# Performance work log

Hardware: AMD Instinct MI355X
Metric: run time of the kernel (lower is better)

## Reference

```python
import jax, jax.numpy as jnp
import numpy as np

B, N, D, E = 256, 192, 512, 1024
H = E // 2          # MLP hidden = 512
K = 58              # round(0.3 * 192), hardcoded in the torch forward
EPS_L2 = 1e-8
EPS_BN = 1e-5


def setup_inputs() -> dict:
    key = jax.random.key(0)
    ks = jax.random.split(key, 8)
    s = 0.02
    return {
        "all_patch_embeddings": jax.random.normal(ks[0], (B, N, D), dtype=jnp.float32),
        "attention_map": jax.random.uniform(ks[1], (B, N + 1, N + 1), dtype=jnp.float32),
        # fc: Linear(D, E)
        "W_fc": jax.random.normal(ks[2], (E, D), dtype=jnp.float32) * s,
        "b_fc": jnp.zeros((E,), dtype=jnp.float32),
        # mlp layer 0: Linear(D, H) + BatchNorm1d(H) + ReLU
        "W1": jax.random.normal(ks[3], (H, D), dtype=jnp.float32) * s,
        "b1": jnp.zeros((H,), dtype=jnp.float32),
        "gamma1": jnp.ones((H,), dtype=jnp.float32),
        "beta1": jnp.zeros((H,), dtype=jnp.float32),
        # mlp layer 1: Linear(H, E) (no BN/ReLU applied on last layer)
        "W2": jax.random.normal(ks[4], (E, H), dtype=jnp.float32) * s,
        "b2": jnp.zeros((E,), dtype=jnp.float32),
    }


def reference(all_patch_embeddings, attention_map, W_fc, b_fc, W1, b1, gamma1, beta1, W2, b2):
    # CLS-row attention over the 192 patch tokens: [B, N]
    cls_attn = attention_map[:, 0, 1:]
    # torch.sort(descending)[...,:K] == top-k indices (batched, replaces python loop)
    _, idx = jax.lax.top_k(cls_attn, K)                      # [B, K] int32
    # batched gather replacing the per-sample index_select loop
    sel = jnp.take_along_axis(all_patch_embeddings, idx[:, :, None], axis=1)  # [B, K, D]
    # l2norm over last dim
    norm = jnp.sqrt(jnp.sum(sel * sel, axis=-1, keepdims=True)) + EPS_L2
    base = sel / norm
    # .half() cast in the original (round-trip to fp16 precision)
    base = base.astype(jnp.float16).astype(jnp.float32)
    # fc branch
    feat_fc = jnp.einsum('bkd,ed->bke', base, W_fc) + b_fc    # [B, K, E]
    # mlp branch (num_layers=2): Linear -> BN(train-mode batch stats) -> ReLU -> Linear
    h = jnp.einsum('bkd,hd->bkh', base, W1) + b1              # [B, K, H]
    hf = h.reshape(B * K, H)
    mu = jnp.mean(hf, axis=0)
    var = jnp.var(hf, axis=0)
    hf = (hf - mu) * jax.lax.rsqrt(var + EPS_BN) * gamma1 + beta1
    h = jax.nn.relu(hf).reshape(B, K, H)
    feat_mlp = jnp.einsum('bkh,eh->bke', h, W2) + b2          # [B, K, E]
    feats = feat_mlp + feat_fc
    # maxk_pool1d_var with k=1 and lengths == K reduces to max over token dim
    return jnp.max(feats, axis=1).astype(jnp.float32)         # [B, E]
```

## Files before the change

kernel.cpp:

```cpp
#include <hip/hip_runtime.h>
#include <hip/hip_fp16.h>

#define B_ 256
#define N_ 192
#define D_ 512
#define E_ 1024
#define H_ 512
#define K_ 58
#define M_ (B_*K_)
#define M2_ (B_*64)

typedef _Float16 f16;
typedef unsigned int u32;
typedef _Float16 half8 __attribute__((ext_vector_type(8)));
typedef float floatx16 __attribute__((ext_vector_type(16)));

__device__ inline half8 cvt8(float4 f0, float4 f1) {
  half8 r;
  r[0]=(f16)f0.x; r[1]=(f16)f0.y; r[2]=(f16)f0.z; r[3]=(f16)f0.w;
  r[4]=(f16)f1.x; r[5]=(f16)f1.y; r[6]=(f16)f1.z; r[7]=(f16)f1.w;
  return r;
}

__device__ inline void gl_lds16(const f16* g, f16* l) {
  __builtin_amdgcn_global_load_lds((const __attribute__((address_space(1))) u32*)g,
                                   (__attribute__((address_space(3))) u32*)l, 16, 0, 0);
}

__device__ inline void stage128(const f16* gbase, int gstride, f16* sT, int w, int lane) {
  int lrow  = lane >> 2;
  int chunk = (lane & 3) ^ ((lane >> 3) & 3);
  gl_lds16(gbase + (size_t)(w*16      + lrow)*gstride + chunk*8, &sT[(w*16)*32]);
  gl_lds16(gbase + (size_t)(64 + w*16 + lrow)*gstride + chunk*8, &sT[(64 + w*16)*32]);
}

__global__ void setup_kernel(const float* __restrict__ Wfc, const float* __restrict__ W2,
                             const float* __restrict__ W1, const float* __restrict__ attn,
                             const float* __restrict__ emb,
                             f16* __restrict__ Wcat, f16* __restrict__ W1_16,
                             f16* __restrict__ A16, float* __restrict__ csum) {
  __shared__ float sv[N_];
  __shared__ int sidx[K_];
  __shared__ int cnt;
  int blk = blockIdx.x, t = threadIdx.x;
  if (blk < 512) {
    int idx = (blk*256 + t)*8;
    int e = idx >> 10, c = idx & 1023;
    const float* src = (c < 512) ? (Wfc + (size_t)e*512 + c)
                                 : (W2  + (size_t)e*512 + (c-512));
    half8 o = cvt8(((const float4*)src)[0], ((const float4*)src)[1]);
    *(uint4*)(Wcat + idx) = *(uint4*)&o;
  } else if (blk < 640) {
    int idx = ((blk-512)*256 + t)*8;
    const float* src = W1 + idx;
    half8 o = cvt8(((const float4*)src)[0], ((const float4*)src)[1]);
    *(uint4*)(W1_16 + idx) = *(uint4*)&o;
  } else if (blk < 896) {
    int b = blk - 640;
    if (t == 0) cnt = 0;
    if (t < N_) sv[t] = attn[(size_t)b*193*193 + 1 + t];
    __syncthreads();
    if (t < N_) {
      float v = sv[t]; int rank = 0;
      for (int j = 0; j < N_; ++j) {
        float vj = sv[j];
        rank += (vj > v) || (vj == v && j < t);
      }
      if (rank < K_) sidx[atomicAdd(&cnt, 1)] = t;
    }
    __syncthreads();
    int w = t >> 6, lane = t & 63;
    for (int slot = w; slot < 64; slot += 4) {
      f16* dst = A16 + ((size_t)b*64 + slot)*1024 + lane*8;
      if (slot < K_) {
        const float* src = emb + ((size_t)b*N_ + sidx[slot])*D_ + lane*8;
        float4 v0 = ((const float4*)src)[0];
        float4 v1 = ((const float4*)src)[1];
        float s = v0.x*v0.x + v0.y*v0.y + v0.z*v0.z + v0.w*v0.w
                + v1.x*v1.x + v1.y*v1.y + v1.z*v1.z + v1.w*v1.w;
        #pragma unroll
        for (int off = 32; off > 0; off >>= 1) s += __shfl_xor(s, off);
        float inv = 1.0f / (sqrtf(s) + 1e-8f);
        half8 o;
        o[0]=(f16)(v0.x*inv); o[1]=(f16)(v0.y*inv); o[2]=(f16)(v0.z*inv); o[3]=(f16)(v0.w*inv);
        o[4]=(f16)(v1.x*inv); o[5]=(f16)(v1.y*inv); o[6]=(f16)(v1.z*inv); o[7]=(f16)(v1.w*inv);
        *(uint4*)dst = *(uint4*)&o;
      } else {
        uint4 z; z.x=0u; z.y=0u; z.z=0u; z.w=0u;
        *(uint4*)dst = z;
      }
    }
  } else {
    float4 z; z.x=0.f; z.y=0.f; z.z=0.f; z.w=0.f;
    ((float4*)csum)[t] = z;
  }
}

__launch_bounds__(256, 2)
__global__ void gemm1_kernel(const f16* __restrict__ A16, const f16* __restrict__ W1_16,
                             const float* __restrict__ b1, f16* __restrict__ Aout,
                             float* __restrict__ csum, float* __restrict__ css) {
  __shared__ f16 sA[2][128*32];
  __shared__ f16 sB[2][128*32];
  __shared__ float sSum[4][64], sSS[4][64];
  int t = threadIdx.x;
  int g = blockIdx.x;
  int xcd = g & 7, rest = g >> 3;
  int n0 = (rest & 3) * 128;
  int m0 = (xcd + 8*(rest >> 2)) * 128;
  int lane = t & 63, w = t >> 6;
  int l31 = lane & 31, khalf = lane >> 5, swz = (l31 >> 1) & 3;
  int rw = w & 1, cw = w >> 1;
  floatx16 acc[2][2] = {};
  const f16* Ab = A16 + (size_t)m0*1024;
  const f16* Bb = W1_16 + (size_t)n0*512;
  stage128(Ab, 1024, sA[0], w, lane);
  stage128(Bb, 512,  sB[0], w, lane);
  __syncthreads();
  for (int it = 0; it < 16; ++it) {
    int cur = it & 1, nxt = cur ^ 1;
    if (it < 15) {
      stage128(Ab + (it+1)*32, 1024, sA[nxt], w, lane);
      stage128(Bb + (it+1)*32, 512,  sB[nxt], w, lane);
    }
    #pragma unroll
    for (int s = 0; s < 2; ++s) {
      int ko = ((s*2 + khalf) ^ swz) * 8;
      half8 a[2], bf[2];
      #pragma unroll
      for (int i = 0; i < 2; ++i) a[i]  = *(const half8*)&sA[cur][(rw*64 + i*32 + l31)*32 + ko];
      #pragma unroll
      for (int j = 0; j < 2; ++j) bf[j] = *(const half8*)&sB[cur][(cw*64 + j*32 + l31)*32 + ko];
      #pragma unroll
      for (int i = 0; i < 2; ++i)
        #pragma unroll
        for (int j = 0; j < 2; ++j)
          acc[i][j] = __builtin_amdgcn_mfma_f32_32x32x16_f16(a[i], bf[j], acc[i][j], 0, 0, 0);
    }
    __syncthreads();
  }
  #pragma unroll
  for (int jt = 0; jt < 2; ++jt) {
    int col = n0 + cw*64 + jt*32 + l31;
    float bias = b1[col];
    float s = 0.f, ss = 0.f;
    #pragma unroll
    for (int i = 0; i < 2; ++i) {
      #pragma unroll
      for (int rg = 0; rg < 16; ++rg) {
        int rib = i*32 + (rg&3) + 8*(rg>>2) + 4*khalf;
        float x = acc[i][jt][rg] + bias;
        Aout[(size_t)(m0 + rw*64 + rib)*1024 + 512 + col] = (f16)x;
        if (i == 0 || rib < K_) { s += x; ss += x*x; }
      }
    }
    s  += __shfl_xor(s, 32);
    ss += __shfl_xor(ss, 32);
    if (lane < 32) { sSum[w][jt*32 + l31] = s; sSS[w][jt*32 + l31] = ss; }
  }
  __syncthreads();
  if (t < 128) {
    int c = t;
    int w0 = 2*(c >> 6), ci = c & 63;
    atomicAdd(&csum[n0 + c], sSum[w0][ci] + sSum[w0+1][ci]);
    atomicAdd(&css[n0 + c],  sSS[w0][ci]  + sSS[w0+1][ci]);
  }
}

__launch_bounds__(256, 3)
__global__ void fused_kernel(const f16* __restrict__ A16, const f16* __restrict__ Wcat,
                             const float* __restrict__ csum, const float* __restrict__ css,
                             const float* __restrict__ gamma, const float* __restrict__ beta,
                             const float* __restrict__ bfc, const float* __restrict__ b2,
                             float* __restrict__ out) {
  __shared__ f16 sA[2][128*32];
  __shared__ f16 sB[2][128*32];
  __shared__ float sSc[H_], sSh[H_];
  __shared__ float sMax[4][64];
  int t = threadIdx.x;
  int g = blockIdx.x;
  int xcd = g & 7, rest = g >> 3;
  int e0 = (rest & 7) * 128;
  int bm = xcd + 8*(rest >> 3);
  int lane = t & 63, w = t >> 6;
  int l31 = lane & 31, khalf = lane >> 5, swz = (l31 >> 1) & 3;
  int rw = w & 1, cw = w >> 1;
  #pragma unroll
  for (int jj = 0; jj < 2; ++jj) {
    int j = t + jj*256;
    float mu  = csum[j] * (1.0f/M_);
    float var = css[j] * (1.0f/M_) - mu*mu;
    float sc  = gamma[j] * rsqrtf(var + 1e-5f);
    sSc[j] = sc;
    sSh[j] = beta[j] - mu*sc;
  }
  floatx16 acc[2][2] = {};
  const f16* Ab = A16 + (size_t)bm*128*1024;
  const f16* Bb = Wcat + (size_t)e0*1024;
  int rr = t >> 2;
  int rslot  = (t & 3) * 8;
  int rchunk = (t & 3) ^ ((t >> 3) & 3);
  bool pad = (rr >= K_);
  stage128(Ab, 1024, sA[0], w, lane);
  stage128(Bb, 1024, sB[0], w, lane);
  __syncthreads();
  for (int it = 0; it < 32; ++it) {
    int cur = it & 1, nxt = cur ^ 1;
    int kn = (it + 1) * 32;
    uint4 h0, h1;
    bool regp = false;
    if (it < 31) {
      stage128(Bb + kn, 1024, sB[nxt], w, lane);
      if (kn < 512) {
        stage128(Ab + kn, 1024, sA[nxt], w, lane);
      } else {
        regp = true;
        const f16* hp = Ab + (size_t)rr*1024 + kn + rchunk*8;
        h0 = *(const uint4*)hp;
        h1 = *(const uint4*)(hp + (size_t)64*1024);
      }
    }
    #pragma unroll
    for (int s = 0; s < 2; ++s) {
      int ko = ((s*2 + khalf) ^ swz) * 8;
      half8 a[2], bf[2];
      #pragma unroll
      for (int i = 0; i < 2; ++i) a[i]  = *(const half8*)&sA[cur][(rw*64 + i*32 + l31)*32 + ko];
      #pragma unroll
      for (int j = 0; j < 2; ++j) bf[j] = *(const half8*)&sB[cur][(cw*64 + j*32 + l31)*32 + ko];
      #pragma unroll
      for (int i = 0; i < 2; ++i)
        #pragma unroll
        for (int j = 0; j < 2; ++j)
          acc[i][j] = __builtin_amdgcn_mfma_f32_32x32x16_f16(a[i], bf[j], acc[i][j], 0, 0, 0);
    }
    if (regp) {
      int cb = kn - 512 + rchunk*8;
      float4 sc0 = *(float4*)&sSc[cb], sc1 = *(float4*)&sSc[cb+4];
      float4 sh0 = *(float4*)&sSh[cb], sh1 = *(float4*)&sSh[cb+4];
      half8 v0 = *(half8*)&h0, v1 = *(half8*)&h1;
      half8 o0, o1;
      o0[0]=(f16)fmaxf((float)v0[0]*sc0.x+sh0.x, 0.f);
      o0[1]=(f16)fmaxf((float)v0[1]*sc0.y+sh0.y, 0.f);
      o0[2]=(f16)fmaxf((float)v0[2]*sc0.z+sh0.z, 0.f);
      o0[3]=(f16)fmaxf((float)v0[3]*sc0.w+sh0.w, 0.f);
      o0[4]=(f16)fmaxf((float)v0[4]*sc1.x+sh1.x, 0.f);
      o0[5]=(f16)fmaxf((float)v0[5]*sc1.y+sh1.y, 0.f);
      o0[6]=(f16)fmaxf((float)v0[6]*sc1.z+sh1.z, 0.f);
      o0[7]=(f16)fmaxf((float)v0[7]*sc1.w+sh1.w, 0.f);
      o1[0]=(f16)fmaxf((float)v1[0]*sc0.x+sh0.x, 0.f);
      o1[1]=(f16)fmaxf((float)v1[1]*sc0.y+sh0.y, 0.f);
      o1[2]=(f16)fmaxf((float)v1[2]*sc0.z+sh0.z, 0.f);
      o1[3]=(f16)fmaxf((float)v1[3]*sc0.w+sh0.w, 0.f);
      o1[4]=(f16)fmaxf((float)v1[4]*sc1.x+sh1.x, 0.f);
      o1[5]=(f16)fmaxf((float)v1[5]*sc1.y+sh1.y, 0.f);
      o1[6]=(f16)fmaxf((float)v1[6]*sc1.z+sh1.z, 0.f);
      o1[7]=(f16)fmaxf((float)v1[7]*sc1.w+sh1.w, 0.f);
      if (pad) {
        uint4 z; z.x=0u; z.y=0u; z.z=0u; z.w=0u;
        *(uint4*)&o0 = z; *(uint4*)&o1 = z;
      }
      *(uint4*)&sA[nxt][rr*32 + rslot]        = *(uint4*)&o0;
      *(uint4*)&sA[nxt][(64 + rr)*32 + rslot] = *(uint4*)&o1;
    }
    __syncthreads();
  }
  #pragma unroll
  for (int jt = 0; jt < 2; ++jt) {
    float mx = -3.0e38f;
    #pragma unroll
    for (int i = 0; i < 2; ++i) {
      #pragma unroll
      for (int rg = 0; rg < 16; ++rg) {
        int rib = i*32 + (rg&3) + 8*(rg>>2) + 4*khalf;
        if (i == 0 || rib < K_) mx = fmaxf(mx, acc[i][jt][rg]);
      }
    }
    mx = fmaxf(mx, __shfl_xor(mx, 32));
    if (lane < 32) sMax[w][jt*32 + l31] = mx;
  }
  __syncthreads();
  #pragma unroll
  for (int bb = 0; bb < 2; ++bb) {
    int c = t & 127;
    if ((t >> 7) == bb) {
      float mx = sMax[bb + 2*(c >> 6)][c & 63];
      int e = e0 + c;
      out[((size_t)bm*2 + bb)*E_ + e] = mx + bfc[e] + b2[e];
    }
  }
}

extern "C" void kernel_launch(void* const* d_in, const int* in_sizes, int n_in,
                              void* d_out, int out_size, void* d_ws, size_t ws_size,
                              hipStream_t stream) {
  const float* emb   = (const float*)d_in[0];
  const float* attn  = (const float*)d_in[1];
  const float* Wfc   = (const float*)d_in[2];
  const float* bfc   = (const float*)d_in[3];
  const float* W1    = (const float*)d_in[4];
  const float* b1    = (const float*)d_in[5];
  const float* gamma = (const float*)d_in[6];
  const float* beta  = (const float*)d_in[7];
  const float* W2    = (const float*)d_in[8];
  const float* b2    = (const float*)d_in[9];
  float* out = (float*)d_out;

  char* ws = (char*)d_ws;
  f16*   A16   = (f16*)(ws);
  f16*   Wcat  = (f16*)(ws + 33554432);
  f16*   W1_16 = (f16*)(ws + 35651584);
  float* csum  = (float*)(ws + 36175872);
  float* css   = (float*)(ws + 36177920);

  setup_kernel<<<897, 256, 0, stream>>>(Wfc, W2, W1, attn, emb, Wcat, W1_16, A16, csum);
  gemm1_kernel<<<512, 256, 0, stream>>>(A16, W1_16, b1, A16, csum, css);
  fused_kernel<<<1024, 256, 0, stream>>>(A16, Wcat, csum, css, gamma, beta, bfc, b2, out);
}
```

Baseline: 239.2 us.

## Restructure fused GEMM to one block per batch with full A tile in LDS

Changes the fused fc+mlp GEMM so each block handles one batch element: the full 64x1024 A row block (embeddings plus BN/ReLU-applied hidden) is staged once into 128KB of dynamic LDS with an XOR swizzle. Each wave then sweeps 256 output columns, reading weights directly from global memory. The aim is to remove repeated A staging and per-iteration synchronisation across column tiles. The cost is one block per CU, no LDS reuse of the weights, and heavy reliance on L2 for B loads. It also launches with a large dynamic shared allocation without setting the function attribute.

```diff
diff --git a/kernel.cpp b/kernel.cpp
--- a/kernel.cpp
+++ b/kernel.cpp
@@ -167,24 +167,18 @@
   }
 }
 
-__launch_bounds__(256, 3)
+__launch_bounds__(256, 1)
 __global__ void fused_kernel(const f16* __restrict__ A16, const f16* __restrict__ Wcat,
                              const float* __restrict__ csum, const float* __restrict__ css,
                              const float* __restrict__ gamma, const float* __restrict__ beta,
                              const float* __restrict__ bfc, const float* __restrict__ b2,
                              float* __restrict__ out) {
-  __shared__ f16 sA[2][128*32];
-  __shared__ f16 sB[2][128*32];
+  extern __shared__ f16 sA[];
   __shared__ float sSc[H_], sSh[H_];
-  __shared__ float sMax[4][64];
   int t = threadIdx.x;
-  int g = blockIdx.x;
-  int xcd = g & 7, rest = g >> 3;
-  int e0 = (rest & 7) * 128;
-  int bm = xcd + 8*(rest >> 3);
+  int b = blockIdx.x;
   int lane = t & 63, w = t >> 6;
-  int l31 = lane & 31, khalf = lane >> 5, swz = (l31 >> 1) & 3;
-  int rw = w & 1, cw = w >> 1;
+  int l31 = lane & 31, khalf = lane >> 5;
   #pragma unroll
   for (int jj = 0; jj < 2; ++jj) {
     int j = t + jj*256;
@@ -194,99 +188,70 @@
     sSc[j] = sc;
     sSh[j] = beta[j] - mu*sc;
   }
-  floatx16 acc[2][2] = {};
-  const f16* Ab = A16 + (size_t)bm*128*1024;
-  const f16* Bb = Wcat + (size_t)e0*1024;
-  int rr = t >> 2;
-  int rslot  = (t & 3) * 8;
-  int rchunk = (t & 3) ^ ((t >> 3) & 3);
-  bool pad = (rr >= K_);
-  stage128(Ab, 1024, sA[0], w, lane);
-  stage128(Bb, 1024, sB[0], w, lane);
-  __syncthreads();
-  for (int it = 0; it < 32; ++it) {
-    int cur = it & 1, nxt = cur ^ 1;
-    int kn = (it + 1) * 32;
-    uint4 h0, h1;
-    bool regp = false;
-    if (it < 31) {
-      stage128(Bb + kn, 1024, sB[nxt], w, lane);
-      if (kn < 512) {
-        stage128(Ab + kn, 1024, sA[nxt], w, lane);
-      } else {
-        regp = true;
-        const f16* hp = Ab + (size_t)rr*1024 + kn + rchunk*8;
-        h0 = *(const uint4*)hp;
-        h1 = *(const uint4*)(hp + (size_t)64*1024);
-      }
-    }
-    #pragma unroll
-    for (int s = 0; s < 2; ++s) {
-      int ko = ((s*2 + khalf) ^ swz) * 8;
-      half8 a[2], bf[2];
-      #pragma unroll
-      for (int i = 0; i < 2; ++i) a[i]  = *(const half8*)&sA[cur][(rw*64 + i*32 + l31)*32 + ko];
-      #pragma unroll
-      for (int j = 0; j < 2; ++j) bf[j] = *(const half8*)&sB[cur][(cw*64 + j*32 + l31)*32 + ko];
-      #pragma unroll
-      for (int i = 0; i < 2; ++i)
-        #pragma unroll
-        for (int j = 0; j < 2; ++j)
-          acc[i][j] = __builtin_amdgcn_mfma_f32_32x32x16_f16(a[i], bf[j], acc[i][j], 0, 0, 0);
-    }
-    if (regp) {
-      int cb = kn - 512 + rchunk*8;
-      float4 sc0 = *(float4*)&sSc[cb], sc1 = *(float4*)&sSc[cb+4];
-      float4 sh0 = *(float4*)&sSh[cb], sh1 = *(float4*)&sSh[cb+4];
-      half8 v0 = *(half8*)&h0, v1 = *(half8*)&h1;
-      half8 o0, o1;
-      o0[0]=(f16)fmaxf((float)v0[0]*sc0.x+sh0.x, 0.f);
-      o0[1]=(f16)fmaxf((float)v0[1]*sc0.y+sh0.y, 0.f);
-      o0[2]=(f16)fmaxf((float)v0[2]*sc0.z+sh0.z, 0.f);
-      o0[3]=(f16)fmaxf((float)v0[3]*sc0.w+sh0.w, 0.f);
-      o0[4]=(f16)fmaxf((float)v0[4]*sc1.x+sh1.x, 0.f);
-      o0[5]=(f16)fmaxf((float)v0[5]*sc1.y+sh1.y, 0.f);
-      o0[6]=(f16)fmaxf((float)v0[6]*sc1.z+sh1.z, 0.f);
-      o0[7]=(f16)fmaxf((float)v0[7]*sc1.w+sh1.w, 0.f);
-      o1[0]=(f16)fmaxf((float)v1[0]*sc0.x+sh0.x, 0.f);
-      o1[1]=(f16)fmaxf((float)v1[1]*sc0.y+sh0.y, 0.f);
-      o1[2]=(f16)fmaxf((float)v1[2]*sc0.z+sh0.z, 0.f);
-      o1[3]=(f16)fmaxf((float)v1[3]*sc0.w+sh0.w, 0.f);
-      o1[4]=(f16)fmaxf((float)v1[4]*sc1.x+sh1.x, 0.f);
-      o1[5]=(f16)fmaxf((float)v1[5]*sc1.y+sh1.y, 0.f);
-      o1[6]=(f16)fmaxf((float)v1[6]*sc1.z+sh1.z, 0.f);
-      o1[7]=(f16)fmaxf((float)v1[7]*sc1.w+sh1.w, 0.f);
-      if (pad) {
-        uint4 z; z.x=0u; z.y=0u; z.z=0u; z.w=0u;
-        *(uint4*)&o0 = z; *(uint4*)&o1 = z;
-      }
-      *(uint4*)&sA[nxt][rr*32 + rslot]        = *(uint4*)&o0;
-      *(uint4*)&sA[nxt][(64 + rr)*32 + rslot] = *(uint4*)&o1;
-    }
-    __syncthreads();
-  }
-  #pragma unroll
-  for (int jt = 0; jt < 2; ++jt) {
-    float mx = -3.0e38f;
-    #pragma unroll
-    for (int i = 0; i < 2; ++i) {
+  __syncthreads();
+  const f16* Ab = A16 + (size_t)b*64*1024;
+  for (int r = w; r < 64; r += 4) {
+    int rx = r & 7;
+    gl_lds16(Ab + (size_t)r*1024 + ((lane ^ rx) * 8), &sA[r*1024]);
+  }
+  {
+    int r  = t & 63;
+    int rx = r & 7;
+    int cb = 64 + (t >> 6) * 16;
+    bool padr = (r >= K_);
+    const f16* hp = Ab + (size_t)r*1024;
+    #pragma unroll
+    for (int q = 0; q < 16; ++q) {
+      int c = cb + q;
+      uint4 hv4 = *(const uint4*)(hp + c*8);
+      half8 hv = *(half8*)&hv4;
+      int j0 = c*8 - 512;
+      half8 o;
+      #pragma unroll
+      for (int i = 0; i < 8; ++i)
+        o[i] = (f16)fmaxf((float)hv[i]*sSc[j0+i] + sSh[j0+i], 0.0f);
+      uint4 ov = *(uint4*)&o;
+      if (padr) { ov.x=0u; ov.y=0u; ov.z=0u; ov.w=0u; }
+      *(uint4*)&sA[r*1024 + (c ^ rx)*8] = ov;
+    }
+  }
+  __syncthreads();
+  int rxl = l31 & 7;
+  int aoff0 = l31*1024;
+  int aoff1 = (32 + l31)*1024;
+  for (int st = 0; st < 4; ++st) {
+    int colbase = w*256 + st*64;
+    const f16* bp0 = Wcat + (size_t)(colbase      + l31)*1024 + khalf*8;
+    const f16* bp1 = Wcat + (size_t)(colbase + 32 + l31)*1024 + khalf*8;
+    floatx16 acc[2][2] = {};
+    #pragma unroll 4
+    for (int ks = 0; ks < 64; ++ks) {
+      int kc = ks*2;
+      int so = ((kc + khalf) ^ rxl) * 8;
+      half8 a0 = *(const half8*)&sA[aoff0 + so];
+      half8 a1 = *(const half8*)&sA[aoff1 + so];
+      half8 b0 = *(const half8*)(bp0 + kc*8);
+      half8 b1v = *(const half8*)(bp1 + kc*8);
+      acc[0][0] = __builtin_amdgcn_mfma_f32_32x32x16_f16(a0, b0,  acc[0][0], 0, 0, 0);
+      acc[0][1] = __builtin_amdgcn_mfma_f32_32x32x16_f16(a0, b1v, acc[0][1], 0, 0, 0);
+      acc[1][0] = __builtin_amdgcn_mfma_f32_32x32x16_f16(a1, b0,  acc[1][0], 0, 0, 0);
+      acc[1][1] = __builtin_amdgcn_mfma_f32_32x32x16_f16(a1, b1v, acc[1][1], 0, 0, 0);
+    }
+    #pragma unroll
+    for (int j = 0; j < 2; ++j) {
+      float mx = -3.0e38f;
+      #pragma unroll
+      for (int rg = 0; rg < 16; ++rg) mx = fmaxf(mx, acc[0][j][rg]);
       #pragma unroll
       for (int rg = 0; rg < 16; ++rg) {
-        int rib = i*32 + (rg&3) + 8*(rg>>2) + 4*khalf;
-        if (i == 0 || rib < K_) mx = fmaxf(mx, acc[i][jt][rg]);
-      }
-    }
-    mx = fmaxf(mx, __shfl_xor(mx, 32));
-    if (lane < 32) sMax[w][jt*32 + l31] = mx;
-  }
-  __syncthreads();
-  #pragma unroll
-  for (int bb = 0; bb < 2; ++bb) {
-    int c = t & 127;
-    if ((t >> 7) == bb) {
-      float mx = sMax[bb + 2*(c >> 6)][c & 63];
-      int e = e0 + c;
-      out[((size_t)bm*2 + bb)*E_ + e] = mx + bfc[e] + b2[e];
+        int rib = 32 + (rg&3) + 8*(rg>>2) + 4*khalf;
+        if (rib < K_) mx = fmaxf(mx, acc[1][j][rg]);
+      }
+      mx = fmaxf(mx, __shfl_xor(mx, 32));
+      if (lane < 32) {
+        int e = colbase + j*32 + l31;
+        out[(size_t)b*E_ + e] = mx + bfc[e] + b2[e];
+      }
     }
   }
 }
@@ -315,5 +280,5 @@
 
   setup_kernel<<<897, 256, 0, stream>>>(Wfc, W2, W1, attn, emb, Wcat, W1_16, A16, csum);
   gemm1_kernel<<<512, 256, 0, stream>>>(A16, W1_16, b1, A16, csum, css);
-  fused_kernel<<<1024, 256, 0, stream>>>(A16, Wcat, csum, css, gamma, beta, bfc, b2, out);
-}
+  fused_kernel<<<256, 256, 131072, stream>>>(A16, Wcat, csum, css, gamma, beta, bfc, b2, out);
+}
```

Result: slower. 273.1 us (+14.2%).
